# Kernel optimization log

Hardware: AMD Instinct MI355X
Metric: run time of the kernel (lower is better)

## Reference

```python
import jax, jax.numpy as jnp
import numpy as np

MIN_LEN = 4      # g.min_word_length
MAX_LEN = 10     # g.max_word_length
THRESH = 0.05    # g.init_threshold
NEG = -1e9


def setup_inputs() -> dict:
    key = jax.random.key(0)
    ks = jax.random.split(key, 6)
    B, L, F, D, U, V = 16, 64, 60, 256, 600, 10000
    x = jax.random.normal(ks[0], (B, L, F), jnp.float32)            # batch dense feat matrix
    unit_feats = jax.random.normal(ks[1], (U, F), jnp.float32)      # per-unit features
    W = jax.random.normal(ks[2], (F, D), jnp.float32) * 0.1         # FeatEmbedding weight
    lengths = jax.random.randint(ks[3], (B,), MIN_LEN, L + 1)       # sentence lengths
    indexed_segments = jax.random.randint(ks[4], (V, MAX_LEN), 0, U)  # vocab -> unit ids
    vocab_length = jax.random.randint(ks[5], (V,), MIN_LEN, MAX_LEN + 1)
    return dict(x=x, unit_feats=unit_feats, W=W, lengths=lengths,
                indexed_segments=indexed_segments, vocab_length=vocab_length)


def reference(x, unit_feats, W, lengths, indexed_segments, vocab_length):
    B, L, _ = x.shape
    V, J = indexed_segments.shape
    # embedding: features -> char_emb space
    word_repr = x @ W                 # [B, L, D]
    unit_repr = unit_feats @ W        # [U, D]
    # cosine similarity between every segment position and every unit
    wn = word_repr / (jnp.linalg.norm(word_repr, axis=-1, keepdims=True) + 1e-8)
    un = unit_repr / (jnp.linalg.norm(unit_repr, axis=-1, keepdims=True) + 1e-8)
    sim = jnp.einsum('bld,ud->blu', wn, un)  # [B, L, U]
    # pad so span gathers past the end read zeros (masked later by `viable`)
    sim_pad = jnp.pad(sim, ((0, 0), (0, J), (0, 0)))
    # accumulate per-position unit scores along each vocab word's unit sequence
    acc = jnp.zeros((B, L, V), sim.dtype)
    per_len = []
    for j in range(J):  # fixed small loop over word-length positions
        # sim at start+j for unit indexed_segments[v, j] -> [B, L, V]
        s_j = sim_pad[:, j:j + L, :][:, :, indexed_segments[:, j]]
        acc = acc + s_j
        if j + 1 >= MIN_LEN:
            per_len.append(acc / (j + 1))  # length-normalized match score
    scores = jnp.stack(per_len, axis=2)  # [B, len_s=L, len_e=E, V]
    E = scores.shape[2]
    k = jnp.arange(E) + MIN_LEN                          # candidate word lengths
    ends = jnp.arange(L)[:, None] + k[None, :] - 1        # [L, E]
    viable = ends[None] < lengths[:, None, None]          # [B, L, E]
    len_match = vocab_length[None, None, None, :] == k[None, None, :, None]
    mask = viable[..., None] & len_match                  # [B, L, E, V]
    masked = jnp.where(mask, scores, NEG)
    # best vocab word per span candidate
    value = masked.max(axis=-1)                           # [B, L, E]
    matched_vocab = masked.argmax(axis=-1)                # [B, L, E]
    matched = value > THRESH
    # best span candidate per batch element (eval path: hard max)
    flat = value.reshape(B, -1)                           # [B, L*E]
    best_inds = flat.argmax(axis=-1)
    best_scores = flat.max(axis=-1)
    best_starts = best_inds // E
    best_ends = best_inds % E + best_starts + MIN_LEN - 1
    any_matched = matched.reshape(B, -1).any(axis=-1)
    best_vocab = jnp.take_along_axis(matched_vocab.reshape(B, -1), best_inds[:, None], axis=1)[:, 0]
    return best_scores, best_starts, best_ends, any_matched, best_vocab
```

## Files before the change

### kernel.cpp

```cpp
#include <hip/hip_runtime.h>
#include <math.h>

#define BB 16
#define LL 64
#define FF 60
#define DD 256
#define UU 600
#define VV 10000
#define JMAX 10
#define MINL 4
#define EE 7
#define NEG (-1e9f)
#define TH 0.05f
#define BCAP 10240

#define UNT_OFF   0
#define WNT_OFF   163840
#define SIM_OFF   425984
#define CNT_OFF   1040384
#define SRT_OFF   1040392
#define VAL_OFF   1613832
#define VOC_OFF   1628168

__global__ __launch_bounds__(256) void k_prep(const int* __restrict__ seg,
                                              const int* __restrict__ vlen,
                                              const float* __restrict__ x,
                                              const float* __restrict__ uf,
                                              const float* __restrict__ W,
                                              unsigned int* __restrict__ cnt,
                                              unsigned int* __restrict__ srt,
                                              float* __restrict__ unT,
                                              float* __restrict__ wnT) {
    int blk = blockIdx.x;
    if (blk < 40) {
        int v = blk * 256 + threadIdx.x;
        if (v >= VV) return;
        int lane = threadIdx.x & 63;
        unsigned long long below = (lane == 0) ? 0ull : (~0ull >> (64 - lane));
        const int* s = seg + v * JMAX;
        unsigned int t[10];
#pragma unroll
        for (int j = 0; j < JMAX; ++j) t[j] = (unsigned int)(s[j] * 13 + j);
        int e = vlen[v] - MINL;
        unsigned int pos = 0;
#pragma unroll
        for (int b2 = 0; b2 < EE; ++b2) {
            unsigned long long m = __ballot(e == b2);
            if (e == b2) {
                int leader = __ffsll((long long)m) - 1;
                unsigned int wc = (unsigned int)__popcll(m);
                unsigned int base = 0;
                if (lane == leader) base = atomicAdd(&cnt[b2], wc);
                base = __shfl(base, leader, 64);
                pos = base + (unsigned int)__popcll(m & below);
            }
        }
        unsigned int* dst = srt + ((size_t)e * BCAP + pos) * 8;
        uint4 qa, qb;
        qa.x = t[0] | (t[1] << 16);
        qa.y = t[2] | (t[3] << 16);
        qa.z = t[4] | (t[5] << 16);
        qa.w = t[6] | (t[7] << 16);
        qb.x = t[8] | (t[9] << 16);
        qb.y = (unsigned int)v;
        qb.z = 0; qb.w = 0;
        ((uint4*)dst)[0] = qa;
        ((uint4*)dst)[1] = qb;
    } else {
        int w = threadIdx.x >> 6;
        int lane = threadIdx.x & 63;
        int id = (blk - 40) * 4 + w;
        const float* row;
        float* outB;
        int stride, col;
        if (id < UU) { row = uf + id * FF; outB = unT; stride = 640;  col = id; }
        else { int bl = id - UU; row = x + bl * FF; outB = wnT; stride = 1024; col = bl; }

        float r0 = 0.f, r1 = 0.f, r2 = 0.f, r3 = 0.f;
#pragma unroll 4
        for (int f = 0; f < FF; ++f) {
            float xv = row[f];
            r0 += xv * W[f * DD + lane];
            r1 += xv * W[f * DD + lane + 64];
            r2 += xv * W[f * DD + lane + 128];
            r3 += xv * W[f * DD + lane + 192];
        }
        float ss = r0 * r0 + r1 * r1 + r2 * r2 + r3 * r3;
#pragma unroll
        for (int m = 32; m > 0; m >>= 1) ss += __shfl_xor(ss, m, 64);
        float inv = 1.0f / (sqrtf(ss) + 1e-8f);
        outB[(lane      ) * stride + col] = r0 * inv;
        outB[(lane +  64) * stride + col] = r1 * inv;
        outB[(lane + 128) * stride + col] = r2 * inv;
        outB[(lane + 192) * stride + col] = r3 * inv;
    }
}

__global__ __launch_bounds__(320) void k_sim(const float* __restrict__ unT,
                                             const float* __restrict__ wnT,
                                             const int* __restrict__ lengths,
                                             float* __restrict__ sim) {
    int blk = blockIdx.x;
    int b  = blk >> 5;
    int r  = blk & 31;
    int l0 = (r >> 1) * 4;
    if (l0 >= lengths[b]) return;
    int uh = r & 1;
    int bl0 = b * 64 + l0;
    int u = uh * 320 + threadIdx.x;

    float a0 = 0.f, a1 = 0.f, a2 = 0.f, a3 = 0.f;
#pragma unroll 8
    for (int d = 0; d < DD; ++d) {
        float4 wv = *(const float4*)(wnT + d * 1024 + bl0);
        float v  = unT[d * 640 + u];
        a0 += wv.x * v;
        a1 += wv.y * v;
        a2 += wv.z * v;
        a3 += wv.w * v;
    }
    if (u < UU) {
        sim[(bl0 + 0) * UU + u] = a0;
        sim[(bl0 + 1) * UU + u] = a1;
        sim[(bl0 + 2) * UU + u] = a2;
        sim[(bl0 + 3) * UU + u] = a3;
    }
}

template<int K>
__device__ __forceinline__ void seg_pass4(const unsigned int* __restrict__ srt,
                                          const float* __restrict__ lds,
                                          int e, int r0, int r1, int lane, int wave,
                                          float (*redS)[8], int (*redV)[8]) {
    float s0 = -1e30f, s1 = -1e30f, s2 = -1e30f, s3 = -1e30f;
    int w0 = VV, w1 = VV, w2 = VV, w3 = VV;
    for (int p = r0 + lane; p < r1; p += 64) {
        const uint4* pp = (const uint4*)(srt + ((size_t)e * BCAP + p) * 8);
        uint4 qa = pp[0];
        uint4 qb = pp[1];
        unsigned int tw[5] = {qa.x, qa.y, qa.z, qa.w, qb.x};
        int v = (int)qb.y;
        float a0 = 0.f, a1 = 0.f, a2 = 0.f, a3 = 0.f;
#pragma unroll
        for (int j = 0; j < K; ++j) {
            int idx = (int)((tw[j >> 1] >> ((j & 1) * 16)) & 0xffffu);
            a0 += lds[idx];
            a1 += lds[idx + 1];
            a2 += lds[idx + 2];
            a3 += lds[idx + 3];
        }
        bool p0 = (a0 > s0) || (a0 == s0 && v < w0);
        bool p1 = (a1 > s1) || (a1 == s1 && v < w1);
        bool p2 = (a2 > s2) || (a2 == s2 && v < w2);
        bool p3 = (a3 > s3) || (a3 == s3 && v < w3);
        s0 = p0 ? a0 : s0;  w0 = p0 ? v : w0;
        s1 = p1 ? a1 : s1;  w1 = p1 ? v : w1;
        s2 = p2 ? a2 : s2;  w2 = p2 ? v : w2;
        s3 = p3 ? a3 : s3;  w3 = p3 ? v : w3;
    }
#pragma unroll
    for (int off = 32; off > 0; off >>= 1) {
        float os; int ov;
        os = __shfl_down(s0, off, 64); ov = __shfl_down(w0, off, 64);
        if (os > s0 || (os == s0 && ov < w0)) { s0 = os; w0 = ov; }
        os = __shfl_down(s1, off, 64); ov = __shfl_down(w1, off, 64);
        if (os > s1 || (os == s1 && ov < w1)) { s1 = os; w1 = ov; }
        os = __shfl_down(s2, off, 64); ov = __shfl_down(w2, off, 64);
        if (os > s2 || (os == s2 && ov < w2)) { s2 = os; w2 = ov; }
        os = __shfl_down(s3, off, 64); ov = __shfl_down(w3, off, 64);
        if (os > s3 || (os == s3 && ov < w3)) { s3 = os; w3 = ov; }
    }
    if (lane == 0) {
        redS[e * 4 + 0][wave] = s0; redV[e * 4 + 0][wave] = w0;
        redS[e * 4 + 1][wave] = s1; redV[e * 4 + 1][wave] = w1;
        redS[e * 4 + 2][wave] = s2; redV[e * 4 + 2][wave] = w2;
        redS[e * 4 + 3][wave] = s3; redV[e * 4 + 3][wave] = w3;
    }
}

__global__ __launch_bounds__(512, 8) void k_score(const float* __restrict__ sim,
                                                  const unsigned int* __restrict__ srt,
                                                  const unsigned int* __restrict__ cnt,
                                                  const int* __restrict__ lengths,
                                                  float* __restrict__ val,
                                                  int* __restrict__ voc) {
    __shared__ float lds[UU * 13];
    __shared__ float redS[28][8];
    __shared__ int   redV[28][8];

    int blk = blockIdx.x;
    int half = blk >> 8;
    int rest = blk & 255;
    int b  = rest >> 4;
    int l0 = (rest & 15) * 4;
    int tid = threadIdx.x;
    int len = lengths[b];

    if (l0 + MINL - 1 >= len) {
        if (tid < 28) {
            int e  = tid >> 2;
            int dl = tid & 3;
            int o = (half * BB * LL + b * 64 + l0 + dl) * EE + e;
            val[o] = NEG;
            voc[o] = 0;
        }
        return;
    }

    if (tid < 224) {
        redS[tid >> 3][tid & 7] = -1e30f;
        redV[tid >> 3][tid & 7] = VV;
    }
    for (int u = tid; u < UU; u += 512) {
#pragma unroll
        for (int r = 0; r < 13; ++r) {
            int m = l0 + r;
            lds[u * 13 + r] = (m < LL) ? sim[(b * 64 + m) * UU + u] : 0.0f;
        }
    }
    __syncthreads();

    int wave = tid >> 6, lane = tid & 63;

    unsigned nlo[EE], nhi[EE], Bw[EE];
    unsigned Wtot = 0;
#pragma unroll
    for (int e = 0; e < EE; ++e) {
        unsigned n = cnt[e];
        unsigned lo = half ? (n >> 1) : 0;
        unsigned hi = half ? n : (n >> 1);
        if (l0 + e + MINL - 1 >= len) { lo = 0; hi = 0; }
        nlo[e] = lo; nhi[e] = hi;
        Bw[e] = Wtot;
        Wtot += (hi - lo) * (unsigned)(e + MINL);
    }
    unsigned qlo = (unsigned)(((unsigned long long)Wtot * (unsigned)wave) >> 3);
    unsigned qhi = (unsigned)(((unsigned long long)Wtot * (unsigned)(wave + 1)) >> 3);

#pragma unroll
    for (int e = 0; e < EE; ++e) {
        unsigned K = (unsigned)(e + MINL);
        unsigned segw = (nhi[e] - nlo[e]) * K;
        unsigned Be = Bw[e];
        if (qhi <= Be || qlo >= Be + segw || segw == 0) continue;
        unsigned a = (qlo > Be) ? (qlo - Be) : 0;
        unsigned bb = qhi - Be; if (bb > segw) bb = segw;
        int r0 = (int)(nlo[e] + (a + K - 1) / K);
        int r1 = (int)(nlo[e] + (bb + K - 1) / K);
        if (r1 <= r0) continue;
        switch (e) {
            case 0: seg_pass4<4> (srt, lds, 0, r0, r1, lane, wave, redS, redV); break;
            case 1: seg_pass4<5> (srt, lds, 1, r0, r1, lane, wave, redS, redV); break;
            case 2: seg_pass4<6> (srt, lds, 2, r0, r1, lane, wave, redS, redV); break;
            case 3: seg_pass4<7> (srt, lds, 3, r0, r1, lane, wave, redS, redV); break;
            case 4: seg_pass4<8> (srt, lds, 4, r0, r1, lane, wave, redS, redV); break;
            case 5: seg_pass4<9> (srt, lds, 5, r0, r1, lane, wave, redS, redV); break;
            case 6: seg_pass4<10>(srt, lds, 6, r0, r1, lane, wave, redS, redV); break;
        }
    }
    __syncthreads();

    if (tid < 28) {
        int e  = tid >> 2;
        int dl = tid & 3;
        float s = redS[tid][0];
        int  vv = redV[tid][0];
#pragma unroll
        for (int w2 = 1; w2 < 8; ++w2) {
            float os = redS[tid][w2];
            int   ov = redV[tid][w2];
            if (os > s || (os == s && ov < vv)) { s = os; vv = ov; }
        }
        int lg = l0 + dl;
        int k = e + MINL;
        bool viable = (lg + k - 1) < len;
        float sn = s / (float)k;
        int o = (half * BB * LL + b * 64 + lg) * EE + e;
        val[o] = viable ? sn : NEG;
        voc[o] = viable ? vv : 0;
    }
}

__global__ __launch_bounds__(512) void k_final(const float* __restrict__ val,
                                               const int* __restrict__ voc,
                                               float* __restrict__ out) {
    __shared__ float sS[8];
    __shared__ int   sI[8];
    __shared__ int   sV[8];
    __shared__ int   sA[8];
    int b = blockIdx.x;
    int t = threadIdx.x;
    float s = -3e38f;
    int idx = 1 << 30;
    int vc = 0;
    int any = 0;
    if (t < LL * EE) {
        int o0 = b * LL * EE + t;
        int o1 = BB * LL * EE + o0;
        float s0 = val[o0], s1 = val[o1];
        int   v0 = voc[o0], v1 = voc[o1];
        bool sel = (s1 > s0) || (s1 == s0 && v1 < v0);
        s  = sel ? s1 : s0;
        vc = sel ? v1 : v0;
        idx = t;
        any = (s > TH) ? 1 : 0;
    }
#pragma unroll
    for (int off = 32; off > 0; off >>= 1) {
        float os = __shfl_down(s, off, 64);
        int   oi = __shfl_down(idx, off, 64);
        int   ov = __shfl_down(vc, off, 64);
        int   oa = __shfl_down(any, off, 64);
        if (os > s || (os == s && oi < idx)) { s = os; idx = oi; vc = ov; }
        any |= oa;
    }
    int w = t >> 6, lane = t & 63;
    if (lane == 0) { sS[w] = s; sI[w] = idx; sV[w] = vc; sA[w] = any; }
    __syncthreads();
    if (t == 0) {
        for (int w2 = 1; w2 < 8; ++w2) {
            float os = sS[w2];
            int   oi = sI[w2];
            if (os > s || (os == s && oi < idx)) { s = os; idx = oi; vc = sV[w2]; }
            any |= sA[w2];
        }
        int start = idx / EE;
        int e = idx - start * EE;
        int end = e + start + MINL - 1;
        out[b]      = s;
        out[16 + b] = (float)start;
        out[32 + b] = (float)end;
        out[48 + b] = any ? 1.0f : 0.0f;
        out[64 + b] = (float)vc;
    }
}

extern "C" void kernel_launch(void* const* d_in, const int* in_sizes, int n_in,
                              void* d_out, int out_size, void* d_ws, size_t ws_size,
                              hipStream_t stream) {
    const float* x       = (const float*)d_in[0];
    const float* uf      = (const float*)d_in[1];
    const float* W       = (const float*)d_in[2];
    const int*   lengths = (const int*)d_in[3];
    const int*   seg     = (const int*)d_in[4];
    const int*   vlen    = (const int*)d_in[5];
    float* out = (float*)d_out;
    float* ws  = (float*)d_ws;

    float*        unT = ws + UNT_OFF;
    float*        wnT = ws + WNT_OFF;
    float*        sim = ws + SIM_OFF;
    unsigned int* cnt = (unsigned int*)(ws + CNT_OFF);
    unsigned int* srt = (unsigned int*)(ws + SRT_OFF);
    float*        val = ws + VAL_OFF;
    int*          voc = (int*)(ws + VOC_OFF);

    hipMemsetAsync(cnt, 0, 8 * sizeof(unsigned int), stream);
    k_prep<<<446, 256, 0, stream>>>(seg, vlen, x, uf, W, cnt, srt, unT, wnT);
    k_sim<<<512, 320, 0, stream>>>(unT, wnT, lengths, sim);
    k_score<<<512, 512, 0, stream>>>(sim, srt, cnt, lengths, val, voc);
    k_final<<<BB, 512, 0, stream>>>(val, voc, out);
}
```

Baseline: 133.3 us.

## Replace atomic bucket counters with deterministic block prefix scan and drop memset

The vocab bucketing in k_prep no longer uses global atomicAdd on counters. Each block recounts the lengths of all earlier vocab entries, packed into 16-bit fields, to get a deterministic base offset per bucket, and block 39 writes the final counts. This removes the hipMemsetAsync launch and gives a stable ordering. It also moves the length normalisation into the score loop so that ties match the reference's divided values. The cost is redundant reads of the vlen array that grow with block index, plus an extra division per candidate in the hot scoring loop.

Result: slower. 155.7 us (+16.8%).

```diff
diff --git a/kernel.cpp b/kernel.cpp
--- a/kernel.cpp
+++ b/kernel.cpp
@@ -31,41 +31,74 @@
                                               unsigned int* __restrict__ srt,
                                               float* __restrict__ unT,
                                               float* __restrict__ wnT) {
+    __shared__ unsigned long long sP[4][2];
+    __shared__ int wTab[4][8];
+    __shared__ int sBase[8];
     int blk = blockIdx.x;
     if (blk < 40) {
-        int v = blk * 256 + threadIdx.x;
-        if (v >= VV) return;
-        int lane = threadIdx.x & 63;
+        int tid  = threadIdx.x;
+        int lane = tid & 63;
+        int w    = tid >> 6;
+        int v    = blk * 256 + tid;
+
+        unsigned long long p0 = 0, p1 = 0;
+        int lim = blk * 256;
+        for (int i = tid; i < lim; i += 256) {
+            int e2 = vlen[i] - MINL;
+            if (e2 < 4) p0 += 1ull << (e2 * 16);
+            else        p1 += 1ull << ((e2 - 4) * 16);
+        }
+#pragma unroll
+        for (int m = 32; m > 0; m >>= 1) {
+            p0 += __shfl_xor(p0, m, 64);
+            p1 += __shfl_xor(p1, m, 64);
+        }
+        if (lane == 0) { sP[w][0] = p0; sP[w][1] = p1; }
+
+        int e = (v < VV) ? (vlen[v] - MINL) : -1;
         unsigned long long below = (lane == 0) ? 0ull : (~0ull >> (64 - lane));
-        const int* s = seg + v * JMAX;
-        unsigned int t[10];
-#pragma unroll
-        for (int j = 0; j < JMAX; ++j) t[j] = (unsigned int)(s[j] * 13 + j);
-        int e = vlen[v] - MINL;
-        unsigned int pos = 0;
+        unsigned long long mym = 0;
 #pragma unroll
         for (int b2 = 0; b2 < EE; ++b2) {
             unsigned long long m = __ballot(e == b2);
-            if (e == b2) {
-                int leader = __ffsll((long long)m) - 1;
-                unsigned int wc = (unsigned int)__popcll(m);
-                unsigned int base = 0;
-                if (lane == leader) base = atomicAdd(&cnt[b2], wc);
-                base = __shfl(base, leader, 64);
-                pos = base + (unsigned int)__popcll(m & below);
-            }
-        }
-        unsigned int* dst = srt + ((size_t)e * BCAP + pos) * 8;
-        uint4 qa, qb;
-        qa.x = t[0] | (t[1] << 16);
-        qa.y = t[2] | (t[3] << 16);
-        qa.z = t[4] | (t[5] << 16);
-        qa.w = t[6] | (t[7] << 16);
-        qb.x = t[8] | (t[9] << 16);
-        qb.y = (unsigned int)v;
-        qb.z = 0; qb.w = 0;
-        ((uint4*)dst)[0] = qa;
-        ((uint4*)dst)[1] = qb;
+            if (lane == 0) wTab[w][b2] = (int)__popcll(m);
+            if (e == b2) mym = m;
+        }
+        __syncthreads();
+        if (tid < EE) {
+            unsigned long long q0 = sP[0][0] + sP[1][0] + sP[2][0] + sP[3][0];
+            unsigned long long q1 = sP[0][1] + sP[1][1] + sP[2][1] + sP[3][1];
+            int base = (tid < 4) ? (int)((q0 >> (tid * 16)) & 0xffffull)
+                                 : (int)((q1 >> ((tid - 4) * 16)) & 0xffffull);
+            sBase[tid] = base;
+            if (blk == 39)
+                cnt[tid] = (unsigned)(base + wTab[0][tid] + wTab[1][tid]
+                                           + wTab[2][tid] + wTab[3][tid]);
+        }
+        __syncthreads();
+
+        if (v < VV) {
+            int prior = sBase[e];
+#pragma unroll
+            for (int w2 = 0; w2 < 4; ++w2) if (w2 < w) prior += wTab[w2][e];
+            unsigned pos = (unsigned)(prior + (int)__popcll(mym & below));
+
+            const int* s = seg + v * JMAX;
+            unsigned int t[10];
+#pragma unroll
+            for (int j = 0; j < JMAX; ++j) t[j] = (unsigned int)(s[j] * 13 + j);
+            unsigned int* dst = srt + ((size_t)e * BCAP + pos) * 8;
+            uint4 qa, qb;
+            qa.x = t[0] | (t[1] << 16);
+            qa.y = t[2] | (t[3] << 16);
+            qa.z = t[4] | (t[5] << 16);
+            qa.w = t[6] | (t[7] << 16);
+            qb.x = t[8] | (t[9] << 16);
+            qb.y = (unsigned int)v;
+            qb.z = 0; qb.w = 0;
+            ((uint4*)dst)[0] = qa;
+            ((uint4*)dst)[1] = qb;
+        }
     } else {
         int w = threadIdx.x >> 6;
         int lane = threadIdx.x & 63;
@@ -149,14 +182,18 @@
             a2 += lds[idx + 2];
             a3 += lds[idx + 3];
         }
-        bool p0 = (a0 > s0) || (a0 == s0 && v < w0);
-        bool p1 = (a1 > s1) || (a1 == s1 && v < w1);
-        bool p2 = (a2 > s2) || (a2 == s2 && v < w2);
-        bool p3 = (a3 > s3) || (a3 == s3 && v < w3);
-        s0 = p0 ? a0 : s0;  w0 = p0 ? v : w0;
-        s1 = p1 ? a1 : s1;  w1 = p1 ? v : w1;
-        s2 = p2 ? a2 : s2;  w2 = p2 ? v : w2;
-        s3 = p3 ? a3 : s3;  w3 = p3 ? v : w3;
+        float n0 = a0 / (float)K;
+        float n1 = a1 / (float)K;
+        float n2 = a2 / (float)K;
+        float n3 = a3 / (float)K;
+        bool p0 = (n0 > s0) || (n0 == s0 && v < w0);
+        bool p1 = (n1 > s1) || (n1 == s1 && v < w1);
+        bool p2 = (n2 > s2) || (n2 == s2 && v < w2);
+        bool p3 = (n3 > s3) || (n3 == s3 && v < w3);
+        s0 = p0 ? n0 : s0;  w0 = p0 ? v : w0;
+        s1 = p1 ? n1 : s1;  w1 = p1 ? v : w1;
+        s2 = p2 ? n2 : s2;  w2 = p2 ? v : w2;
+        s3 = p3 ? n3 : s3;  w3 = p3 ? v : w3;
     }
 #pragma unroll
     for (int off = 32; off > 0; off >>= 1) {
@@ -274,9 +311,8 @@
         int lg = l0 + dl;
         int k = e + MINL;
         bool viable = (lg + k - 1) < len;
-        float sn = s / (float)k;
         int o = (half * BB * LL + b * 64 + lg) * EE + e;
-        val[o] = viable ? sn : NEG;
+        val[o] = viable ? s : NEG;
         voc[o] = viable ? vv : 0;
     }
 }
@@ -355,7 +391,6 @@
     float*        val = ws + VAL_OFF;
     int*          voc = (int*)(ws + VOC_OFF);
 
-    hipMemsetAsync(cnt, 0, 8 * sizeof(unsigned int), stream);
     k_prep<<<446, 256, 0, stream>>>(seg, vlen, x, uf, W, cnt, srt, unT, wnT);
     k_sim<<<512, 320, 0, stream>>>(unT, wnT, lengths, sim);
     k_score<<<512, 512, 0, stream>>>(sim, srt, cnt, lengths, val, voc);
```
